# Performance work log

Measured on AMD Instinct MI355X. Metric: run time of the kernel, lower is better.

The kernel has to match this reference:

```python
import jax, jax.numpy as jnp
import numpy as np

N_NODES = 50000
N_RELATIONS = 8


def _rgcn_layer(x, src, dst, etype, W, root, bias):
    # PyG RGCNConv (aggr='mean'): out[n] = sum_r mean_{(s->n) in rel r} x[s] @ W[r] + x[n] @ root + bias
    N, d = x.shape
    R = W.shape[0]
    seg = etype * N + dst                                  # combined (relation, dst) segment id
    msg = x[src]                                           # [E, d] gather
    agg = jax.ops.segment_sum(msg, seg, num_segments=R * N)
    cnt = jax.ops.segment_sum(jnp.ones((src.shape[0],), x.dtype), seg, num_segments=R * N)
    agg = agg / jnp.maximum(cnt, 1.0)[:, None]             # mean aggregation (0 if no edges)
    agg = agg.reshape(R, N, d)
    return jnp.einsum('rnd,rdh->nh', agg, W) + x @ root + bias


def setup_inputs() -> dict:
    key = jax.random.key(0)
    ks = jax.random.split(key, 10)
    d_in, d_hid, d_out = 128, 128, 64
    E = 800000
    x = jax.random.normal(ks[0], (N_NODES, d_in), dtype=jnp.float32)
    edge_index = jax.random.randint(ks[1], (2, E), 0, N_NODES, dtype=jnp.int64)
    edge_type = jax.random.randint(ks[2], (E,), 0, N_RELATIONS, dtype=jnp.int64)
    s = 0.05
    W1 = jax.random.normal(ks[3], (N_RELATIONS, d_in, d_hid), dtype=jnp.float32) * s
    root1 = jax.random.normal(ks[4], (d_in, d_hid), dtype=jnp.float32) * s
    bias1 = jnp.zeros((d_hid,), dtype=jnp.float32)
    W2 = jax.random.normal(ks[5], (N_RELATIONS, d_hid, d_out), dtype=jnp.float32) * s
    root2 = jax.random.normal(ks[6], (d_hid, d_out), dtype=jnp.float32) * s
    bias2 = jnp.zeros((d_out,), dtype=jnp.float32)
    return {"x": x, "edge_index": edge_index, "edge_type": edge_type,
            "W1": W1, "root1": root1, "bias1": bias1,
            "W2": W2, "root2": root2, "bias2": bias2}


def reference(x, edge_index, edge_type, W1, root1, bias1, W2, root2, bias2):
    src, dst = edge_index[0], edge_index[1]
    h = _rgcn_layer(x, src, dst, edge_type, W1, root1, bias1)
    h = jax.nn.relu(h)
    out = _rgcn_layer(h, src, dst, edge_type, W2, root2, bias2)
    return out
```

## Files before the change

kernel.cpp:

```cpp
#include <hip/hip_runtime.h>
#include <hip/hip_bf16.h>


#define D_IN 128
#define NREL 8

typedef short bf16x8 __attribute__((ext_vector_type(8)));
typedef float f32x4 __attribute__((ext_vector_type(4)));

__device__ __forceinline__ ushort cvbf(float f) {
    unsigned u = __float_as_uint(f);
    return (ushort)((u + 0x7FFFu + ((u >> 16) & 1u)) >> 16);
}
__device__ __forceinline__ float bflo(unsigned v) { return __uint_as_float(v << 16); }
__device__ __forceinline__ float bfhi(unsigned v) { return __uint_as_float(v & 0xFFFF0000u); }

__global__ void prep_kernel(const float* __restrict__ x, ushort* __restrict__ xb,
                            int n4x,
                            const float* __restrict__ W1,
                            const float* __restrict__ root1,
                            ushort* __restrict__ wt1,
                            const float* __restrict__ W2,
                            const float* __restrict__ root2,
                            ushort* __restrict__ wt2) {
    int i = blockIdx.x * blockDim.x + threadIdx.x;
    if (i < n4x) {
        float4 v = ((const float4*)x)[i];
        ushort4 o;
        o.x = cvbf(v.x); o.y = cvbf(v.y); o.z = cvbf(v.z); o.w = cvbf(v.w);
        ((ushort4*)xb)[i] = o;
        return;
    }
    int j = i - n4x;
    constexpr int TOT1 = (NREL + 1) * D_IN * 128;
    constexpr int TOT2 = (NREL + 1) * D_IN * 64;
    if (j < TOT1) {
        int s = j / (D_IN * 128);
        int r = j - s * (D_IN * 128);
        int k = r / 128;
        int n = r - k * 128;
        float v = (s < NREL) ? W1[(size_t)s * D_IN * 128 + (size_t)k * 128 + n]
                             : root1[(size_t)k * 128 + n];
        int byteoff = (k << 1) ^ ((n & 7) << 4);
        wt1[(size_t)s * 128 * D_IN + (size_t)n * D_IN + (byteoff >> 1)] = cvbf(v);
        return;
    }
    j -= TOT1;
    if (j < TOT2) {
        int s = j / (D_IN * 64);
        int r = j - s * (D_IN * 64);
        int k = r / 64;
        int n = r - k * 64;
        float v = (s < NREL) ? W2[(size_t)s * D_IN * 64 + (size_t)k * 64 + n]
                             : root2[(size_t)k * 64 + n];
        int byteoff = (k << 1) ^ ((n & 7) << 4);
        wt2[(size_t)s * 64 * D_IN + (size_t)n * D_IN + (byteoff >> 1)] = cvbf(v);
    }
}

__global__ void count_kernel(const int* __restrict__ dst,
                             const int* __restrict__ et,
                             int* __restrict__ cnt, int E, int N) {
    int e = blockIdx.x * blockDim.x + threadIdx.x;
    if (e < E) atomicAdd(&cnt[et[e] * N + dst[e]], 1);
}

__global__ void scan_block_sum(const int* __restrict__ cnt,
                               int* __restrict__ bsum, int nseg) {
    __shared__ int s[256];
    int base = blockIdx.x * 1024 + threadIdx.x * 4;
    int v = 0;
#pragma unroll
    for (int i = 0; i < 4; ++i) {
        int idx = base + i;
        if (idx < nseg) v += cnt[idx];
    }
    s[threadIdx.x] = v;
    __syncthreads();
    for (int off = 128; off > 0; off >>= 1) {
        if (threadIdx.x < off) s[threadIdx.x] += s[threadIdx.x + off];
        __syncthreads();
    }
    if (threadIdx.x == 0) bsum[blockIdx.x] = s[0];
}

__global__ void scan_bsum(int* __restrict__ bsum, int nb) {
    __shared__ int s[512];
    int t = threadIdx.x;
    int my = (t < nb) ? bsum[t] : 0;
    s[t] = my;
    __syncthreads();
    for (int off = 1; off < 512; off <<= 1) {
        int v = (t >= off) ? s[t - off] : 0;
        __syncthreads();
        s[t] += v;
        __syncthreads();
    }
    if (t < nb) bsum[t] = s[t] - my;
}

__global__ void scan_write(const int* __restrict__ cnt,
                           const int* __restrict__ bsum,
                           int* __restrict__ off, int nseg) {
    __shared__ int s[256];
    int t = threadIdx.x;
    int base = blockIdx.x * 1024 + t * 4;
    int v[4];
    int sum = 0;
#pragma unroll
    for (int i = 0; i < 4; ++i) {
        int idx = base + i;
        v[i] = (idx < nseg) ? cnt[idx] : 0;
        sum += v[i];
    }
    s[t] = sum;
    __syncthreads();
    int my = sum;
    for (int o = 1; o < 256; o <<= 1) {
        int x = (t >= o) ? s[t - o] : 0;
        __syncthreads();
        s[t] += x;
        __syncthreads();
    }
    int pre = s[t] - my + bsum[blockIdx.x];
#pragma unroll
    for (int i = 0; i < 4; ++i) {
        int idx = base + i;
        if (idx < nseg) {
            off[idx] = pre;
            pre += v[i];
        }
    }
}

__global__ void bucket_kernel(const int* __restrict__ src,
                              const int* __restrict__ dst,
                              const int* __restrict__ et,
                              int* __restrict__ off,
                              ushort* __restrict__ sids, int E, int N) {
    int e = blockIdx.x * blockDim.x + threadIdx.x;
    if (e < E) {
        int seg = et[e] * N + dst[e];
        int pos = atomicAdd(&off[seg], 1);
        sids[pos] = (ushort)src[e];
    }
}

__global__ __launch_bounds__(256) void aggregate_kernel(
    const ushort* __restrict__ feat,
    const ushort* __restrict__ sids,
    const int* __restrict__ endoff,
    ushort* __restrict__ agg,
    int nseg) {
    int gid = blockIdx.x * blockDim.x + threadIdx.x;
    int s = gid >> 4;
    int l = gid & 15;
    if (s >= nseg) return;
    int gbase = threadIdx.x & 48;

    int end = endoff[s];
    int start = (s == 0) ? 0 : endoff[s - 1];
    int deg = end - start;

    float a0 = 0.f, a1 = 0.f, a2 = 0.f, a3 = 0.f;
    float a4 = 0.f, a5 = 0.f, a6 = 0.f, a7 = 0.f;
    for (int base = start; base < end; base += 16) {
        int m = min(16, end - base);
        int sid = (l < m) ? (int)sids[base + l] : 0;
#pragma unroll 2
        for (int j = 0; j < m; ++j) {
            int id = __shfl(sid, gbase + j);
            uint4 v = ((const uint4*)(feat + (size_t)id * D_IN))[l];
            a0 += bflo(v.x); a1 += bfhi(v.x);
            a2 += bflo(v.y); a3 += bfhi(v.y);
            a4 += bflo(v.z); a5 += bfhi(v.z);
            a6 += bflo(v.w); a7 += bfhi(v.w);
        }
    }
    float inv = (deg > 0) ? 1.0f / (float)deg : 0.0f;
    uint4 o;
    o.x = (unsigned)cvbf(a0 * inv) | ((unsigned)cvbf(a1 * inv) << 16);
    o.y = (unsigned)cvbf(a2 * inv) | ((unsigned)cvbf(a3 * inv) << 16);
    o.z = (unsigned)cvbf(a4 * inv) | ((unsigned)cvbf(a5 * inv) << 16);
    o.w = (unsigned)cvbf(a6 * inv) | ((unsigned)cvbf(a7 * inv) << 16);
    ((uint4*)(agg + (size_t)s * D_IN))[l] = o;
}

template <int NCOLS, bool RELU, bool OUTBF16>
__global__ __launch_bounds__(256) void mfma_gemm_kernel(
    const ushort* __restrict__ feat,
    const ushort* __restrict__ agg,
    const ushort* __restrict__ Wt,
    const float* __restrict__ bias,
    void* __restrict__ outp,
    int N) {
    constexpr int NT = NCOLS / 16;
    __shared__ ushort Bt[NCOLS * D_IN];

    const int tid = threadIdx.x;
    const int wave = tid >> 6;
    const int lane = tid & 63;
    const int c = lane & 15;
    const int g = lane >> 4;
    const int rb = blockIdx.x * 64 + wave * 16;
    const int arow = min(rb + c, N - 1);

    f32x4 acc[NT];
#pragma unroll
    for (int t = 0; t < NT; ++t) acc[t] = (f32x4){0.f, 0.f, 0.f, 0.f};

    for (int s = 0; s < NREL + 1; ++s) {
        const ushort* Aseg = (s < NREL) ? (agg + (size_t)s * N * D_IN) : feat;
        {
            const uint4* srcw = (const uint4*)(Wt + (size_t)s * NCOLS * D_IN);
            uint4* dstw = (uint4*)Bt;
#pragma unroll
            for (int i = 0; i < (NCOLS * D_IN) / (8 * 256); ++i)
                dstw[tid + i * 256] = srcw[tid + i * 256];
        }
        __syncthreads();
        const ushort* Abase = Aseg + (size_t)arow * D_IN + 8 * g;
#pragma unroll
        for (int kt = 0; kt < D_IN; kt += 32) {
            bf16x8 a = *(const bf16x8*)(Abase + kt);
#pragma unroll
            for (int t = 0; t < NT; ++t) {
                int n = t * 16 + c;
                int byteoff = n * 256 + ((kt * 2 + g * 16) ^ ((n & 7) << 4));
                bf16x8 b = *(const bf16x8*)((const char*)Bt + byteoff);
                acc[t] = __builtin_amdgcn_mfma_f32_16x16x32_bf16(a, b, acc[t], 0, 0, 0);
            }
        }
        __syncthreads();
    }

#pragma unroll
    for (int t = 0; t < NT; ++t) {
        float bv = bias[t * 16 + c];
#pragma unroll
        for (int r = 0; r < 4; ++r) {
            int orow = rb + 4 * g + r;
            if (orow < N) {
                float v = acc[t][r] + bv;
                if (RELU) v = fmaxf(v, 0.0f);
                if (OUTBF16)
                    ((ushort*)outp)[(size_t)orow * NCOLS + t * 16 + c] = cvbf(v);
                else
                    ((float*)outp)[(size_t)orow * NCOLS + t * 16 + c] = v;
            }
        }
    }
}

__global__ __launch_bounds__(256) void mfma_gemm_db_kernel(
    const ushort* __restrict__ feat,
    const ushort* __restrict__ agg,
    const ushort* __restrict__ Wt,
    const float* __restrict__ bias,
    float* __restrict__ outp,
    int N) {
    constexpr int NCOLS = 64;
    constexpr int NT = 4;
    __shared__ ushort Bt[2][NCOLS * D_IN];

    const int tid = threadIdx.x;
    const int wave = tid >> 6;
    const int lane = tid & 63;
    const int c = lane & 15;
    const int g = lane >> 4;
    const int rb = blockIdx.x * 64 + wave * 16;
    const int arow = min(rb + c, N - 1);
    const size_t aoff = (size_t)arow * D_IN + 8 * g;

#define STAGE2(S, BUF)                                                        \
    do {                                                                      \
        const uint4* srcw = (const uint4*)(Wt + (size_t)(S)*NCOLS * D_IN);    \
        uint4* dstw = (uint4*)(Bt[(BUF)]);                                    \
        _Pragma("unroll") for (int i = 0; i < (NCOLS * D_IN) / (8 * 256); ++i)\
            dstw[tid + i * 256] = srcw[tid + i * 256];                        \
    } while (0)

    f32x4 acc[NT];
#pragma unroll
    for (int t = 0; t < NT; ++t) acc[t] = (f32x4){0.f, 0.f, 0.f, 0.f};

    STAGE2(0, 0);
    __syncthreads();

    for (int s = 0; s < NREL + 1; ++s) {
        const int cur = s & 1;
        if (s < NREL) STAGE2(s + 1, cur ^ 1);
        const ushort* Aseg = (s < NREL) ? (agg + (size_t)s * N * D_IN) : feat;
        const ushort* ab = Aseg + aoff;
        const char* bt = (const char*)(Bt[cur]);
#pragma unroll
        for (int kt = 0; kt < D_IN; kt += 32) {
            bf16x8 a = *(const bf16x8*)(ab + kt);
#pragma unroll
            for (int t = 0; t < NT; ++t) {
                int n = t * 16 + c;
                int byteoff = n * 256 + ((kt * 2 + g * 16) ^ ((n & 7) << 4));
                bf16x8 b = *(const bf16x8*)(bt + byteoff);
                acc[t] = __builtin_amdgcn_mfma_f32_16x16x32_bf16(a, b, acc[t], 0, 0, 0);
            }
        }
        __syncthreads();
    }

#pragma unroll
    for (int t = 0; t < NT; ++t) {
        float bv = bias[t * 16 + c];
#pragma unroll
        for (int r = 0; r < 4; ++r) {
            int orow = rb + 4 * g + r;
            if (orow < N)
                outp[(size_t)orow * NCOLS + t * 16 + c] = acc[t][r] + bv;
        }
    }
#undef STAGE2
}

extern "C" void kernel_launch(void* const* d_in, const int* in_sizes, int n_in,
                              void* d_out, int out_size, void* d_ws, size_t ws_size,
                              hipStream_t stream) {
    const float* x = (const float*)d_in[0];
    const int* ei = (const int*)d_in[1];
    const int* et = (const int*)d_in[2];
    const float* W1 = (const float*)d_in[3];
    const float* root1 = (const float*)d_in[4];
    const float* bias1 = (const float*)d_in[5];
    const float* W2 = (const float*)d_in[6];
    const float* root2 = (const float*)d_in[7];
    const float* bias2 = (const float*)d_in[8];
    float* out = (float*)d_out;

    const int N = in_sizes[0] / D_IN;
    const int E = in_sizes[2];
    const int* src = ei;
    const int* dst = ei + E;
    const int NSEG = NREL * N;
    const int NB = (NSEG + 1023) / 1024;

    ushort* aggb = (ushort*)d_ws;
    ushort* xb = aggb + (size_t)NSEG * D_IN;
    ushort* hb = xb + (size_t)N * D_IN;
    ushort* wt1 = hb + (size_t)N * D_IN;
    ushort* wt2 = wt1 + (size_t)(NREL + 1) * D_IN * D_IN;
    ushort* sids = wt2 + (size_t)(NREL + 1) * 64 * D_IN;
    int* off = (int*)(sids + E);
    int* cnt = off + NSEG;
    int* bsum = cnt + NSEG;

    const int n4x = N * D_IN / 4;
    const int prepTot = n4x + (NREL + 1) * D_IN * 128 + (NREL + 1) * D_IN * 64;
    prep_kernel<<<(prepTot + 255) / 256, 256, 0, stream>>>(
        x, xb, n4x, W1, root1, wt1, W2, root2, wt2);

    hipMemsetAsync(cnt, 0, (size_t)NSEG * sizeof(int), stream);
    count_kernel<<<(E + 255) / 256, 256, 0, stream>>>(dst, et, cnt, E, N);
    scan_block_sum<<<NB, 256, 0, stream>>>(cnt, bsum, NSEG);
    scan_bsum<<<1, 512, 0, stream>>>(bsum, NB);
    scan_write<<<NB, 256, 0, stream>>>(cnt, bsum, off, NSEG);
    bucket_kernel<<<(E + 255) / 256, 256, 0, stream>>>(src, dst, et, off, sids, E, N);

    const int aggBlocks = (int)(((size_t)NSEG * 16 + 255) / 256);
    const int gemmBlocks = (N + 63) / 64;

    aggregate_kernel<<<aggBlocks, 256, 0, stream>>>(xb, sids, off, aggb, NSEG);
    mfma_gemm_kernel<128, true, true><<<gemmBlocks, 256, 0, stream>>>(
        xb, aggb, wt1, bias1, hb, N);

    aggregate_kernel<<<aggBlocks, 256, 0, stream>>>(hb, sids, off, aggb, NSEG);
    mfma_gemm_db_kernel<<<gemmBlocks, 256, 0, stream>>>(
        hb, aggb, wt2, bias2, out, N);
}
```

Before: 251.8 us.

## Replace CSR count/scan/bucket build with atomic linked-list per segment

Swaps the CSR construction (count, three-kernel prefix scan, bucket) for a single kernel that builds per-segment linked lists with atomicExch on a head array. Each list node stores the next edge index and the source id. The aggregate kernel now walks the chain instead of reading a contiguous id range. This removes four launches and the scan passes, but each edge step in aggregation becomes a dependent pointer-chasing load with random access and 8-byte nodes, which serialises memory latency.

```diff
diff --git a/kernel.cpp b/kernel.cpp
--- a/kernel.cpp
+++ b/kernel.cpp
@@ -58,124 +58,43 @@
     }
 }
 
-__global__ void count_kernel(const int* __restrict__ dst,
-                             const int* __restrict__ et,
-                             int* __restrict__ cnt, int E, int N) {
-    int e = blockIdx.x * blockDim.x + threadIdx.x;
-    if (e < E) atomicAdd(&cnt[et[e] * N + dst[e]], 1);
-}
-
-__global__ void scan_block_sum(const int* __restrict__ cnt,
-                               int* __restrict__ bsum, int nseg) {
-    __shared__ int s[256];
-    int base = blockIdx.x * 1024 + threadIdx.x * 4;
-    int v = 0;
-#pragma unroll
-    for (int i = 0; i < 4; ++i) {
-        int idx = base + i;
-        if (idx < nseg) v += cnt[idx];
-    }
-    s[threadIdx.x] = v;
-    __syncthreads();
-    for (int off = 128; off > 0; off >>= 1) {
-        if (threadIdx.x < off) s[threadIdx.x] += s[threadIdx.x + off];
-        __syncthreads();
-    }
-    if (threadIdx.x == 0) bsum[blockIdx.x] = s[0];
-}
-
-__global__ void scan_bsum(int* __restrict__ bsum, int nb) {
-    __shared__ int s[512];
-    int t = threadIdx.x;
-    int my = (t < nb) ? bsum[t] : 0;
-    s[t] = my;
-    __syncthreads();
-    for (int off = 1; off < 512; off <<= 1) {
-        int v = (t >= off) ? s[t - off] : 0;
-        __syncthreads();
-        s[t] += v;
-        __syncthreads();
-    }
-    if (t < nb) bsum[t] = s[t] - my;
-}
-
-__global__ void scan_write(const int* __restrict__ cnt,
-                           const int* __restrict__ bsum,
-                           int* __restrict__ off, int nseg) {
-    __shared__ int s[256];
-    int t = threadIdx.x;
-    int base = blockIdx.x * 1024 + t * 4;
-    int v[4];
-    int sum = 0;
-#pragma unroll
-    for (int i = 0; i < 4; ++i) {
-        int idx = base + i;
-        v[i] = (idx < nseg) ? cnt[idx] : 0;
-        sum += v[i];
-    }
-    s[t] = sum;
-    __syncthreads();
-    int my = sum;
-    for (int o = 1; o < 256; o <<= 1) {
-        int x = (t >= o) ? s[t - o] : 0;
-        __syncthreads();
-        s[t] += x;
-        __syncthreads();
-    }
-    int pre = s[t] - my + bsum[blockIdx.x];
-#pragma unroll
-    for (int i = 0; i < 4; ++i) {
-        int idx = base + i;
-        if (idx < nseg) {
-            off[idx] = pre;
-            pre += v[i];
-        }
-    }
-}
-
-__global__ void bucket_kernel(const int* __restrict__ src,
-                              const int* __restrict__ dst,
-                              const int* __restrict__ et,
-                              int* __restrict__ off,
-                              ushort* __restrict__ sids, int E, int N) {
+__global__ void build_list_kernel(const int* __restrict__ src,
+                                  const int* __restrict__ dst,
+                                  const int* __restrict__ et,
+                                  int* __restrict__ head,
+                                  int2* __restrict__ list, int E, int N) {
     int e = blockIdx.x * blockDim.x + threadIdx.x;
     if (e < E) {
         int seg = et[e] * N + dst[e];
-        int pos = atomicAdd(&off[seg], 1);
-        sids[pos] = (ushort)src[e];
+        int prev = atomicExch(&head[seg], e);
+        list[e] = make_int2(prev, src[e]);
     }
 }
 
 __global__ __launch_bounds__(256) void aggregate_kernel(
     const ushort* __restrict__ feat,
-    const ushort* __restrict__ sids,
-    const int* __restrict__ endoff,
+    const int2* __restrict__ list,
+    const int* __restrict__ head,
     ushort* __restrict__ agg,
     int nseg) {
     int gid = blockIdx.x * blockDim.x + threadIdx.x;
     int s = gid >> 4;
     int l = gid & 15;
     if (s >= nseg) return;
-    int gbase = threadIdx.x & 48;
-
-    int end = endoff[s];
-    int start = (s == 0) ? 0 : endoff[s - 1];
-    int deg = end - start;
-
+
+    int e = head[s];
+    int deg = 0;
     float a0 = 0.f, a1 = 0.f, a2 = 0.f, a3 = 0.f;
     float a4 = 0.f, a5 = 0.f, a6 = 0.f, a7 = 0.f;
-    for (int base = start; base < end; base += 16) {
-        int m = min(16, end - base);
-        int sid = (l < m) ? (int)sids[base + l] : 0;
-#pragma unroll 2
-        for (int j = 0; j < m; ++j) {
-            int id = __shfl(sid, gbase + j);
-            uint4 v = ((const uint4*)(feat + (size_t)id * D_IN))[l];
-            a0 += bflo(v.x); a1 += bfhi(v.x);
-            a2 += bflo(v.y); a3 += bfhi(v.y);
-            a4 += bflo(v.z); a5 += bfhi(v.z);
-            a6 += bflo(v.w); a7 += bfhi(v.w);
-        }
+    while (e >= 0) {
+        int2 p = list[e];
+        ++deg;
+        uint4 v = ((const uint4*)(feat + (size_t)p.y * D_IN))[l];
+        a0 += bflo(v.x); a1 += bfhi(v.x);
+        a2 += bflo(v.y); a3 += bfhi(v.y);
+        a4 += bflo(v.z); a5 += bfhi(v.z);
+        a6 += bflo(v.w); a7 += bfhi(v.w);
+        e = p.x;
     }
     float inv = (deg > 0) ? 1.0f / (float)deg : 0.0f;
     uint4 o;
@@ -252,7 +171,7 @@
     }
 }
 
-__global__ __launch_bounds__(256) void mfma_gemm_db_kernel(
+__global__ void __launch_bounds__(256) mfma_gemm_db_kernel(
     const ushort* __restrict__ feat,
     const ushort* __restrict__ agg,
     const ushort* __restrict__ Wt,
@@ -339,38 +258,32 @@
     const int* src = ei;
     const int* dst = ei + E;
     const int NSEG = NREL * N;
-    const int NB = (NSEG + 1023) / 1024;
 
     ushort* aggb = (ushort*)d_ws;
     ushort* xb = aggb + (size_t)NSEG * D_IN;
     ushort* hb = xb + (size_t)N * D_IN;
     ushort* wt1 = hb + (size_t)N * D_IN;
     ushort* wt2 = wt1 + (size_t)(NREL + 1) * D_IN * D_IN;
-    ushort* sids = wt2 + (size_t)(NREL + 1) * 64 * D_IN;
-    int* off = (int*)(sids + E);
-    int* cnt = off + NSEG;
-    int* bsum = cnt + NSEG;
+    int* head = (int*)(wt2 + (size_t)(NREL + 1) * 64 * D_IN);
+    int2* list = (int2*)(head + NSEG);
 
     const int n4x = N * D_IN / 4;
     const int prepTot = n4x + (NREL + 1) * D_IN * 128 + (NREL + 1) * D_IN * 64;
     prep_kernel<<<(prepTot + 255) / 256, 256, 0, stream>>>(
         x, xb, n4x, W1, root1, wt1, W2, root2, wt2);
 
-    hipMemsetAsync(cnt, 0, (size_t)NSEG * sizeof(int), stream);
-    count_kernel<<<(E + 255) / 256, 256, 0, stream>>>(dst, et, cnt, E, N);
-    scan_block_sum<<<NB, 256, 0, stream>>>(cnt, bsum, NSEG);
-    scan_bsum<<<1, 512, 0, stream>>>(bsum, NB);
-    scan_write<<<NB, 256, 0, stream>>>(cnt, bsum, off, NSEG);
-    bucket_kernel<<<(E + 255) / 256, 256, 0, stream>>>(src, dst, et, off, sids, E, N);
+    hipMemsetAsync(head, 0xFF, (size_t)NSEG * sizeof(int), stream);
+    build_list_kernel<<<(E + 255) / 256, 256, 0, stream>>>(
+        src, dst, et, head, list, E, N);
 
     const int aggBlocks = (int)(((size_t)NSEG * 16 + 255) / 256);
     const int gemmBlocks = (N + 63) / 64;
 
-    aggregate_kernel<<<aggBlocks, 256, 0, stream>>>(xb, sids, off, aggb, NSEG);
+    aggregate_kernel<<<aggBlocks, 256, 0, stream>>>(xb, list, head, aggb, NSEG);
     mfma_gemm_kernel<128, true, true><<<gemmBlocks, 256, 0, stream>>>(
         xb, aggb, wt1, bias1, hb, N);
 
-    aggregate_kernel<<<aggBlocks, 256, 0, stream>>>(hb, sids, off, aggb, NSEG);
+    aggregate_kernel<<<aggBlocks, 256, 0, stream>>>(hb, list, head, aggb, NSEG);
     mfma_gemm_db_kernel<<<gemmBlocks, 256, 0, stream>>>(
         hb, aggb, wt2, bias2, out, N);
 }
```

Measured after the change: 228.8 us. -9.1%, faster.
